# Kernel tuning notes

Measured on AMD Instinct MI355X. Metric: run time of the kernel, lower is better.

## Reference

```python
import jax, jax.numpy as jnp
import numpy as np
from jax import lax

B, M, T = 64, 90, 187
NNLS_ITERS = 500   # fixed-iteration FISTA projected-gradient NNLS (replaces scipy.optimize.nnls loop)
POWER_ITERS = 50
NEG = 0.33         # leaky_relu negative_slope in BrainNetCNN


def leaky(x):
    return jnp.where(x >= 0, x, NEG * x)


def setup_inputs() -> dict:
    key = jax.random.key(0)
    ks = jax.random.split(key, 18)
    f32 = jnp.float32
    def g(k, shape, scale=0.05):
        return jax.random.normal(k, shape, dtype=f32) * scale
    return {
        "x0_raw": jax.random.normal(ks[0], (B, M, T), dtype=f32),   # trunk output res0+res2
        "raw_x": jax.random.normal(ks[1], (B, M, T), dtype=f32),    # mel[:, 0]
        # BrainNetCNN(1, 90, 2) parameters (full-extent conv kernels stored without singleton dims)
        "cnn1_w": g(ks[2], (8, M)),   "cnn1_b": jnp.zeros((8,), f32),    # Conv2d(1,8,(1,90))
        "cnn2_w": g(ks[3], (8, M)),   "cnn2_b": jnp.zeros((8,), f32),    # Conv2d(1,8,(90,1))
        "cnn3_w": g(ks[4], (16, 8, M)), "cnn3_b": jnp.zeros((16,), f32), # Conv2d(8,16,(1,90))
        "cnn4_w": g(ks[5], (16, 8, M)), "cnn4_b": jnp.zeros((16,), f32), # Conv2d(8,16,(90,1))
        "e2n_w": g(ks[6], (16, M)),  "e2n_b": jnp.zeros((1,), f32),      # Conv2d(16,1,(1,90))
        "n2g_w": g(ks[7], (64, M)),  "n2g_b": jnp.zeros((64,), f32),     # Conv2d(1,64,(90,1))
        "d1_w": g(ks[8], (128, 64)), "d1_b": jnp.zeros((128,), f32),
        "d2_w": g(ks[9], (10, 128)), "d2_b": jnp.zeros((10,), f32),
        "d3_w": g(ks[10], (2, 10)),  "d3_b": jnp.zeros((2,), f32),
    }


def nnls_columns(x0_pred, raw_x):
    """Batched NNLS: for each (b, j) solve min_{w>=0} ||X[:, !=j] w - raw_x[b, j]||^2.
    X = x0_pred^T [B,T,M]. Column j is excluded via a mask (its coefficient is pinned to 0),
    which is equivalent to deleting the column. Returns A[b, j, m] with zero diagonal
    (matching torch: A[i, indx, j] = nnls(...); A = A.transpose(1,2))."""
    X = jnp.swapaxes(x0_pred, 1, 2)                    # [B,T,M]
    G = jnp.einsum('btm,btn->bmn', X, X)               # [B,M,M] Gram, shared over all j-problems
    C = jnp.einsum('btm,bjt->bjm', X, raw_x)           # [B,M(j),M] X^T b_j
    mask = 1.0 - jnp.eye(M, dtype=X.dtype)             # mask[j,m]: exclude column j
    # Lipschitz constant: top eigenvalue of G via power iteration (valid bound for masked subproblems)
    v = jnp.ones((G.shape[0], M), G.dtype)
    def pit(v, _):
        v = jnp.einsum('bmn,bn->bm', G, v)
        v = v / (jnp.linalg.norm(v, axis=1, keepdims=True) + 1e-12)
        return v, None
    v, _ = lax.scan(pit, v, None, length=POWER_ITERS)
    L = jnp.einsum('bm,bmn,bn->b', v, G, v) * 1.01 + 1e-8
    step = (1.0 / L)[:, None, None]
    w0 = jnp.zeros_like(C)
    def fista(carry, _):
        w, y, t = carry
        grad = (jnp.einsum('bmn,bjn->bjm', G, y) - C) * mask
        w1 = jnp.maximum(y - step * grad, 0.0)
        t1 = 0.5 * (1.0 + jnp.sqrt(1.0 + 4.0 * t * t))
        y1 = w1 + ((t - 1.0) / t1) * (w1 - w)
        return (w1, y1, t1), None
    (w, _, _), _ = lax.scan(fista, (w0, w0, jnp.float32(1.0)), None, length=NNLS_ITERS)
    return w  # [B, j, m], diag == 0


def brainnet_cnn(A, cnn1_w, cnn1_b, cnn2_w, cnn2_b, cnn3_w, cnn3_b, cnn4_w, cnn4_b,
                 e2n_w, e2n_b, n2g_w, n2g_b, d1_w, d1_b, d2_w, d2_b, d3_w, d3_b):
    # E2E layer 1: row conv broadcast over width + col conv broadcast over height
    a = jnp.einsum('bhw,ow->boh', A, cnn1_w) + cnn1_b[None, :, None]   # [B,8,90]
    b = jnp.einsum('bhw,oh->bow', A, cnn2_w) + cnn2_b[None, :, None]   # [B,8,90]
    o1 = leaky(a[:, :, :, None] + b[:, :, None, :])                    # [B,8,90,90]
    a2 = jnp.einsum('bchw,ocw->boh', o1, cnn3_w) + cnn3_b[None, :, None]
    b2 = jnp.einsum('bchw,och->bow', o1, cnn4_w) + cnn4_b[None, :, None]
    o2 = leaky(a2[:, :, :, None] + b2[:, :, None, :])                  # [B,16,90,90]
    e2n = leaky(jnp.einsum('bchw,cw->bh', o2, e2n_w) + e2n_b)          # [B,90]
    n2g = leaky(jnp.einsum('bh,oh->bo', e2n, n2g_w) + n2g_b)           # [B,64]
    h = leaky(n2g @ d1_w.T + d1_b)
    h = leaky(h @ d2_w.T + d2_b)
    return leaky(h @ d3_w.T + d3_b)                                    # [B,2]


def reference(x0_raw, raw_x, cnn1_w, cnn1_b, cnn2_w, cnn2_b, cnn3_w, cnn3_b, cnn4_w, cnn4_b,
              e2n_w, e2n_b, n2g_w, n2g_b, d1_w, d1_b, d2_w, d2_b, d3_w, d3_b):
    mean_v = jnp.mean(x0_raw, axis=(1, 2), keepdims=True)
    max_v = jnp.max(jnp.abs(x0_raw), axis=(1, 2), keepdims=True)
    x0_pred = (x0_raw - mean_v) / max_v
    # torch detaches NNLS inputs (.detach().numpy()); mirror with stop_gradient
    A = nnls_columns(lax.stop_gradient(x0_pred), lax.stop_gradient(raw_x))
    cls_pred = brainnet_cnn(A, cnn1_w, cnn1_b, cnn2_w, cnn2_b, cnn3_w, cnn3_b, cnn4_w, cnn4_b,
                            e2n_w, e2n_b, n2g_w, n2g_b, d1_w, d1_b, d2_w, d2_b, d3_w, d3_b)
    return (x0_pred[:, None, :, :], A, cls_pred)
```

## Files before the change

### kernel.cpp

```cpp
#include <hip/hip_runtime.h>
#include <math.h>


#define B_ 64
#define M_ 90
#define T_ 187
#define MP 96
#define NNLS_ITERS 500
#define POWER_ITERS 50
#define NEG_SLOPE 0.33f

#define MT_ (M_ * T_)
#define X0_OFF 0
#define A_OFF (B_ * MT_)
#define CLS_OFF (A_OFF + B_ * M_ * M_)

#define WS_G 0
#define WS_C (B_ * MP * MP)
#define WS_STEP (2 * B_ * MP * MP)
#define WS_W3R (WS_STEP + B_)
#define WS_W4R (WS_W3R + 16 * 8 * M_)

typedef float f32x4 __attribute__((ext_vector_type(4)));
typedef short s16x8 __attribute__((ext_vector_type(8)));

__device__ __forceinline__ float leaky(float x) {
    return x >= 0.f ? x : NEG_SLOPE * x;
}

__global__ __launch_bounds__(256) void k_norm(const float* __restrict__ x0,
                                              float* __restrict__ out) {
    int b = blockIdx.x, tid = threadIdx.x;
    const float* x = x0 + b * MT_;
    float s = 0.f, mx = 0.f;
    for (int i = tid; i < MT_; i += 256) {
        float v = x[i];
        s += v;
        mx = fmaxf(mx, fabsf(v));
    }
    __shared__ float rs[256], rm[256];
    rs[tid] = s; rm[tid] = mx;
    __syncthreads();
    for (int st = 128; st > 0; st >>= 1) {
        if (tid < st) {
            rs[tid] += rs[tid + st];
            rm[tid] = fmaxf(rm[tid], rm[tid + st]);
        }
        __syncthreads();
    }
    float mean = rs[0] / (float)MT_;
    float mv = rm[0];
    float* o = out + X0_OFF + b * MT_;
    for (int i = tid; i < MT_; i += 256) {
        o[i] = (x[i] - mean) / mv;
    }
}

#define TSTR 193
__global__ __launch_bounds__(256) void k_gc(const float* __restrict__ out_x0,
                                            const float* __restrict__ rawx,
                                            float* __restrict__ ws) {
    int b = blockIdx.x, nh = blockIdx.y, tid = threadIdx.x;
    __shared__ float Ps[MP * TSTR];
    __shared__ float Rs[48 * TSTR];

    for (int i = tid; i < MP * TSTR; i += 256) Ps[i] = 0.f;
    for (int i = tid; i < 48 * TSTR; i += 256) Rs[i] = 0.f;
    __syncthreads();

    const float* P = out_x0 + X0_OFF + b * MT_;
    const float* R = rawx + b * MT_;
    for (int i = tid; i < MT_; i += 256) {
        int m = i / T_, t = i - m * T_;
        Ps[m * TSTR + t] = P[i];
    }
    for (int i = tid; i < 48 * T_; i += 256) {
        int k = i / T_, t = i - k * T_;
        int r = nh * 48 + k;
        if (r < M_) Rs[k * TSTR + t] = R[r * T_ + t];
    }
    __syncthreads();

    int tn = tid & 15;
    int tm = tid >> 4;
    const float* pmp = &Ps[(tm * 6) * TSTR];
    const float* pnp = &Ps[(nh * 48 + tn * 3) * TSTR];
    const float* rnp = &Rs[(tn * 3) * TSTR];

    float accG[6][3], accC[6][3];
#pragma unroll
    for (int i = 0; i < 6; ++i)
#pragma unroll
        for (int k = 0; k < 3; ++k) { accG[i][k] = 0.f; accC[i][k] = 0.f; }

#pragma unroll 2
    for (int t = 0; t < T_; ++t) {
        float pm[6], pn[3], rn[3];
#pragma unroll
        for (int i = 0; i < 6; ++i) pm[i] = pmp[i * TSTR + t];
#pragma unroll
        for (int k = 0; k < 3; ++k) { pn[k] = pnp[k * TSTR + t]; rn[k] = rnp[k * TSTR + t]; }
#pragma unroll
        for (int i = 0; i < 6; ++i)
#pragma unroll
            for (int k = 0; k < 3; ++k) {
                accG[i][k] = fmaf(pm[i], pn[k], accG[i][k]);
                accC[i][k] = fmaf(pm[i], rn[k], accC[i][k]);
            }
    }

    float* G = ws + WS_G + b * MP * MP;
    float* C = ws + WS_C + b * MP * MP;
#pragma unroll
    for (int i = 0; i < 6; ++i)
#pragma unroll
        for (int k = 0; k < 3; ++k) {
            int m = tm * 6 + i;
            int n = nh * 48 + tn * 3 + k;
            G[m * MP + n] = accG[i][k];
            C[n * MP + m] = accC[i][k];
        }
}

__global__ __launch_bounds__(256) void k_prepack(const float* __restrict__ w3,
                                                 const float* __restrict__ w4,
                                                 float* __restrict__ ws) {
    int tid = threadIdx.x + blockIdx.x * 256;
    for (int i = tid; i < 16 * 8 * M_; i += 512) {
        int o = i & 15;
        int cw = i >> 4;
        int c = cw / M_;
        int w = cw % M_;
        ws[WS_W3R + i] = w3[(o * 8 + c) * M_ + w];
        ws[WS_W4R + i] = w4[(o * 8 + c) * M_ + w];
    }
}

#define GSTR 100
__global__ __launch_bounds__(64) void k_power(float* __restrict__ ws) {
    int b = blockIdx.x, lane = threadIdx.x;
    const float* Gg = ws + WS_G + b * MP * MP;
    __shared__ float Gs[MP * GSTR];
    __shared__ float vs[MP];

    for (int i = lane; i < MP * MP; i += 64) {
        int m = i / MP, n = i - m * MP;
        Gs[m * GSTR + n] = Gg[i];
    }
    vs[lane] = (lane < M_) ? 1.f : 0.f;
    if (lane < 32) vs[64 + lane] = (64 + lane < M_) ? 1.f : 0.f;

    const float4* g0 = (const float4*)&Gs[lane * GSTR];
    const float4* g1 = (const float4*)&Gs[(64 + (lane & 31)) * GSTR];
    const float4* v4 = (const float4*)vs;

    float r0 = 0.f, r1 = 0.f;
    for (int it = 0; it <= POWER_ITERS; ++it) {
        r0 = 0.f; r1 = 0.f;
#pragma unroll 6
        for (int k = 0; k < MP / 4; ++k) {
            float4 gv = g0[k];
            float4 vv = v4[k];
            r0 = fmaf(gv.x, vv.x, r0);
            r0 = fmaf(gv.y, vv.y, r0);
            r0 = fmaf(gv.z, vv.z, r0);
            r0 = fmaf(gv.w, vv.w, r0);
        }
        if (lane < 32) {
#pragma unroll 6
            for (int k = 0; k < MP / 4; ++k) {
                float4 gv = g1[k];
                float4 vv = v4[k];
                r1 = fmaf(gv.x, vv.x, r1);
                r1 = fmaf(gv.y, vv.y, r1);
                r1 = fmaf(gv.z, vv.z, r1);
                r1 = fmaf(gv.w, vv.w, r1);
            }
        }
        if (it == POWER_ITERS) break;
        float s = r0 * r0 + ((lane < 32) ? r1 * r1 : 0.f);
#pragma unroll
        for (int d = 1; d < 64; d <<= 1) s += __shfl_xor(s, d, 64);
        float inv = 1.f / (sqrtf(s) + 1e-12f);
        vs[lane] = r0 * inv;
        if (lane < 32) vs[64 + lane] = r1 * inv;
    }
    float s = vs[lane] * r0 + ((lane < 32) ? vs[64 + lane] * r1 : 0.f);
#pragma unroll
    for (int d = 1; d < 64; d <<= 1) s += __shfl_xor(s, d, 64);
    if (lane == 0) ws[WS_STEP + b] = 1.f / (s * 1.01f + 1e-8f);
}

#define YSTR 104

__global__ __launch_bounds__(192) void k_fista(const float* __restrict__ ws,
                                               float* __restrict__ out) {
    int b = blockIdx.y;
    int j0 = blockIdx.x * 16;
    int tid = threadIdx.x;
    int wid = tid >> 6;
    int lane = tid & 63;
    int jl = lane & 15;
    int g = lane >> 4;

    const float* Gg = ws + WS_G + b * MP * MP;
    const float* Cg = ws + WS_C + b * MP * MP;
    float step = ws[WS_STEP + b];

    __shared__ unsigned short Yt[2][2][16 * YSTR];

    for (int i = tid; i < 2 * 2 * 16 * YSTR / 2; i += 192)
        ((unsigned int*)Yt)[i] = 0u;

    s16x8 ghi[2][3], glo[2][3];
#pragma unroll
    for (int ml = 0; ml < 2; ++ml)
#pragma unroll
        for (int nc = 0; nc < 3; ++nc) {
            const float* src = Gg + ((wid * 2 + ml) * 16 + jl) * MP + nc * 32 + g * 8;
            s16x8 h, l;
#pragma unroll
            for (int e = 0; e < 8; ++e) {
                float f = src[e];
                unsigned int hb = __float_as_uint(f) & 0xFFFF0000u;
                h[e] = (short)(hb >> 16);
                float lo = f - __uint_as_float(hb);
                l[e] = (short)(__float_as_uint(lo) >> 16);
            }
            ghi[ml][nc] = h;
            glo[ml][nc] = l;
        }

    float c[2][4], w[2][4], y[2][4];
#pragma unroll
    for (int ml = 0; ml < 2; ++ml) {
        const float* src = Cg + (j0 + jl) * MP + (wid * 2 + ml) * 16 + g * 4;
#pragma unroll
        for (int r = 0; r < 4; ++r) {
            c[ml][r] = src[r];
            w[ml][r] = 0.f;
            y[ml][r] = 0.f;
        }
    }

    const unsigned short* rb[2][2];
    unsigned short* wb[2][2];
#pragma unroll
    for (int bu = 0; bu < 2; ++bu)
#pragma unroll
        for (int hl = 0; hl < 2; ++hl) {
            rb[bu][hl] = &Yt[bu][hl][jl * YSTR + g * 8];
            wb[bu][hl] = &Yt[bu][hl][jl * YSTR + wid * 32 + g * 4];
        }

    float t = 1.f;
    __syncthreads();

#define FISTA_BODY(CUR, NXT)                                                   \
    {                                                                          \
        s16x8 yh[3], yl[3];                                                    \
        _Pragma("unroll")                                                      \
        for (int nc = 0; nc < 3; ++nc) {                                       \
            yh[nc] = *(const s16x8*)(rb[CUR][0] + nc * 32);                    \
            yl[nc] = *(const s16x8*)(rb[CUR][1] + nc * 32);                    \
        }                                                                      \
        float t1 = 0.5f * (1.f + sqrtf(1.f + 4.f * t * t));                    \
        float coef = (t - 1.f) / t1;                                           \
        t = t1;                                                                \
        _Pragma("unroll")                                                      \
        for (int ml = 0; ml < 2; ++ml) {                                       \
            f32x4 a1 = {0.f, 0.f, 0.f, 0.f}, a2 = {0.f, 0.f, 0.f, 0.f};        \
            _Pragma("unroll")                                                  \
            for (int nc = 0; nc < 3; ++nc)                                     \
                a1 = __builtin_amdgcn_mfma_f32_16x16x32_bf16(ghi[ml][nc], yh[nc], a1, 0, 0, 0); \
            _Pragma("unroll")                                                  \
            for (int nc = 0; nc < 3; ++nc) {                                   \
                a2 = __builtin_amdgcn_mfma_f32_16x16x32_bf16(ghi[ml][nc], yl[nc], a2, 0, 0, 0); \
                a2 = __builtin_amdgcn_mfma_f32_16x16x32_bf16(glo[ml][nc], yh[nc], a2, 0, 0, 0); \
            }                                                                  \
            unsigned int hb[4], lb[4];                                         \
            _Pragma("unroll")                                                  \
            for (int r = 0; r < 4; ++r) {                                      \
                int mg = (wid * 2 + ml) * 16 + g * 4 + r;                      \
                float gr = (a1[r] + a2[r]) - c[ml][r];                         \
                if (j0 + jl == mg) gr = 0.f;                                   \
                float w1v = fmaxf(fmaf(-step, gr, y[ml][r]), 0.f);             \
                float yn = fmaf(coef, w1v - w[ml][r], w1v);                    \
                w[ml][r] = w1v;                                                \
                y[ml][r] = yn;                                                 \
                hb[r] = __float_as_uint(yn) & 0xFFFF0000u;                     \
                float lo = yn - __uint_as_float(hb[r]);                        \
                lb[r] = __float_as_uint(lo);                                   \
            }                                                                  \
            unsigned int h0 = (hb[0] >> 16) | hb[1];                           \
            unsigned int h1 = (hb[2] >> 16) | hb[3];                           \
            unsigned int l0 = (lb[0] >> 16) | (lb[1] & 0xFFFF0000u);           \
            unsigned int l1 = (lb[2] >> 16) | (lb[3] & 0xFFFF0000u);           \
            *(uint2*)(wb[NXT][0] + ml * 16) = make_uint2(h0, h1);              \
            *(uint2*)(wb[NXT][1] + ml * 16) = make_uint2(l0, l1);              \
        }                                                                      \
        __syncthreads();                                                       \
    }

    for (int it = 0; it < NNLS_ITERS / 2; ++it) {
        FISTA_BODY(0, 1)
        FISTA_BODY(1, 0)
    }
#undef FISTA_BODY

    int jg = j0 + jl;
#pragma unroll
    for (int ml = 0; ml < 2; ++ml)
#pragma unroll
        for (int r = 0; r < 4; ++r) {
            int mg = (wid * 2 + ml) * 16 + g * 4 + r;
            if (jg < M_ && mg < M_)
                out[A_OFF + b * M_ * M_ + jg * M_ + mg] = w[ml][r];
        }
}

__global__ __launch_bounds__(256) void k_cnn(
    const float* __restrict__ out_in, const float* __restrict__ ws,
    const float* __restrict__ c1w, const float* __restrict__ c1b,
    const float* __restrict__ c2w, const float* __restrict__ c2b,
    const float* __restrict__ c3b, const float* __restrict__ c4b,
    const float* __restrict__ e2nw, const float* __restrict__ e2nb,
    const float* __restrict__ n2gw, const float* __restrict__ n2gb,
    const float* __restrict__ d1w, const float* __restrict__ d1b,
    const float* __restrict__ d2w, const float* __restrict__ d2b,
    const float* __restrict__ d3w, const float* __restrict__ d3b,
    float* __restrict__ out) {
    int b = blockIdx.x, tid = threadIdx.x;
    __shared__ float A[M_][92];
    __shared__ float a1[8][92], b1[8][92];
    __shared__ float a2s[16][92], b2s[16][92];
    __shared__ float part[16][92];
    __shared__ float e2n[92], n2g[64], h1[128], h2[12];

    const float* Ag = out_in + A_OFF + b * M_ * M_;
    for (int i = tid; i < M_ * M_; i += 256) A[i / M_][i % M_] = Ag[i];
    __syncthreads();

    for (int q = tid; q < 8 * M_; q += 256) {
        int o = q & 7, h = q >> 3;
        float s = c1b[o];
#pragma unroll 2
        for (int wI = 0; wI < M_; ++wI) s = fmaf(A[h][wI], c1w[o * M_ + wI], s);
        a1[o][h] = s;
    }
    for (int q = tid; q < 8 * M_; q += 256) {
        int o = q & 7, wI = q >> 3;
        float s = c2b[o];
#pragma unroll 2
        for (int h = 0; h < M_; ++h) s = fmaf(A[h][wI], c2w[o * M_ + h], s);
        b1[o][wI] = s;
    }
    __syncthreads();

    const float4* w3r4 = (const float4*)(ws + WS_W3R);
    const float4* w4r4 = (const float4*)(ws + WS_W4R);
    for (int q = tid; q < 720; q += 256) {
        if (q < 360) {
            int oq = q & 3, h = q >> 2;
            float4 acc = make_float4(c3b[4 * oq], c3b[4 * oq + 1],
                                     c3b[4 * oq + 2], c3b[4 * oq + 3]);
#pragma unroll
            for (int ci = 0; ci < 8; ++ci) {
                float av = a1[ci][h];
                for (int wI = 0; wI < M_; ++wI) {
                    float o1v = leaky(av + b1[ci][wI]);
                    float4 wv = w3r4[(ci * M_ + wI) * 4 + oq];
                    acc.x = fmaf(o1v, wv.x, acc.x);
                    acc.y = fmaf(o1v, wv.y, acc.y);
                    acc.z = fmaf(o1v, wv.z, acc.z);
                    acc.w = fmaf(o1v, wv.w, acc.w);
                }
            }
            a2s[4 * oq + 0][h] = acc.x;
            a2s[4 * oq + 1][h] = acc.y;
            a2s[4 * oq + 2][h] = acc.z;
            a2s[4 * oq + 3][h] = acc.w;
        } else {
            int q2 = q - 360;
            int oq = q2 & 3, wI = q2 >> 2;
            float4 acc = make_float4(c4b[4 * oq], c4b[4 * oq + 1],
                                     c4b[4 * oq + 2], c4b[4 * oq + 3]);
#pragma unroll
            for (int ci = 0; ci < 8; ++ci) {
                float bv = b1[ci][wI];
                for (int h = 0; h < M_; ++h) {
                    float o1v = leaky(a1[ci][h] + bv);
                    float4 wv = w4r4[(ci * M_ + h) * 4 + oq];
                    acc.x = fmaf(o1v, wv.x, acc.x);
                    acc.y = fmaf(o1v, wv.y, acc.y);
                    acc.z = fmaf(o1v, wv.z, acc.z);
                    acc.w = fmaf(o1v, wv.w, acc.w);
                }
            }
            b2s[4 * oq + 0][wI] = acc.x;
            b2s[4 * oq + 1][wI] = acc.y;
            b2s[4 * oq + 2][wI] = acc.z;
            b2s[4 * oq + 3][wI] = acc.w;
        }
    }
    __syncthreads();

    for (int q = tid; q < 16 * M_; q += 256) {
        int ci = q & 15, h = q >> 4;
        float av = a2s[ci][h];
        float s = 0.f;
        for (int wI = 0; wI < M_; ++wI)
            s = fmaf(leaky(av + b2s[ci][wI]), e2nw[ci * M_ + wI], s);
        part[ci][h] = s;
    }
    __syncthreads();
    if (tid < M_) {
        float s = e2nb[0];
#pragma unroll
        for (int ci = 0; ci < 16; ++ci) s += part[ci][tid];
        e2n[tid] = leaky(s);
    }
    __syncthreads();
    if (tid < 64) {
        float s = n2gb[tid];
        for (int h = 0; h < M_; ++h) s = fmaf(e2n[h], n2gw[tid * M_ + h], s);
        n2g[tid] = leaky(s);
    }
    __syncthreads();
    if (tid < 128) {
        float s = d1b[tid];
        for (int k = 0; k < 64; ++k) s = fmaf(n2g[k], d1w[tid * 64 + k], s);
        h1[tid] = leaky(s);
    }
    __syncthreads();
    if (tid < 10) {
        float s = d2b[tid];
        for (int k = 0; k < 128; ++k) s = fmaf(h1[k], d2w[tid * 128 + k], s);
        h2[tid] = leaky(s);
    }
    __syncthreads();
    if (tid < 2) {
        float s = d3b[tid];
        for (int k = 0; k < 10; ++k) s = fmaf(h2[k], d3w[tid * 10 + k], s);
        out[CLS_OFF + b * 2 + tid] = leaky(s);
    }
}

extern "C" void kernel_launch(void* const* d_in, const int* in_sizes, int n_in,
                              void* d_out, int out_size, void* d_ws, size_t ws_size,
                              hipStream_t stream) {
    const float* x0 = (const float*)d_in[0];
    const float* rawx = (const float*)d_in[1];
    const float* c1w = (const float*)d_in[2];
    const float* c1b = (const float*)d_in[3];
    const float* c2w = (const float*)d_in[4];
    const float* c2b = (const float*)d_in[5];
    const float* c3w = (const float*)d_in[6];
    const float* c3b = (const float*)d_in[7];
    const float* c4w = (const float*)d_in[8];
    const float* c4b = (const float*)d_in[9];
    const float* e2nw = (const float*)d_in[10];
    const float* e2nb = (const float*)d_in[11];
    const float* n2gw = (const float*)d_in[12];
    const float* n2gb = (const float*)d_in[13];
    const float* d1w = (const float*)d_in[14];
    const float* d1b = (const float*)d_in[15];
    const float* d2w = (const float*)d_in[16];
    const float* d2b = (const float*)d_in[17];
    const float* d3w = (const float*)d_in[18];
    const float* d3b = (const float*)d_in[19];

    float* out = (float*)d_out;
    float* ws = (float*)d_ws;

    hipLaunchKernelGGL(k_norm, dim3(B_), dim3(256), 0, stream, x0, out);
    hipLaunchKernelGGL(k_gc, dim3(B_, 2), dim3(256), 0, stream, out, rawx, ws);
    hipLaunchKernelGGL(k_prepack, dim3(2), dim3(256), 0, stream, c3w, c4w, ws);
    hipLaunchKernelGGL(k_power, dim3(B_), dim3(64), 0, stream, ws);
    hipLaunchKernelGGL(k_fista, dim3(MP / 16, B_), dim3(192), 0, stream, ws, out);
    hipLaunchKernelGGL(k_cnn, dim3(B_), dim3(256), 0, stream, out, ws,
                       c1w, c1b, c2w, c2b, c3b, c4b, e2nw, e2nb,
                       n2gw, n2gb, d1w, d1b, d2w, d2b, d3w, d3b, out);
}
```

Measured before the change: 724.7 us.

## Fuse normalization into Gram kernel and split FISTA rows across six waves

Folds the per-batch normalization kernel into the Gram/cross-product kernel: each block recomputes the mean and max itself, and only the first column-half block writes x0_pred. This removes one launch and a global round-trip. The FISTA kernel now runs with 384 threads, so each wave owns a single 16-row tile instead of two. That halves the serial MFMA chain per iteration and splits the error-compensation MFMAs into three independent accumulators, in exchange for redundant reduction work and more waves contending at each per-iteration barrier.

```diff
diff --git a/kernel.cpp b/kernel.cpp
--- a/kernel.cpp
+++ b/kernel.cpp
@@ -28,18 +28,26 @@
     return x >= 0.f ? x : NEG_SLOPE * x;
 }
 
-__global__ __launch_bounds__(256) void k_norm(const float* __restrict__ x0,
-                                              float* __restrict__ out) {
-    int b = blockIdx.x, tid = threadIdx.x;
+#define TSTR 193
+__global__ __launch_bounds__(256) void k_gc(const float* __restrict__ x0,
+                                            const float* __restrict__ rawx,
+                                            float* __restrict__ ws,
+                                            float* __restrict__ out) {
+    int b = blockIdx.x, nh = blockIdx.y, tid = threadIdx.x;
+    __shared__ float Ps[MP * TSTR];
+    __shared__ float Rs[48 * TSTR];
+    __shared__ float rs[256], rm[256];
+
     const float* x = x0 + b * MT_;
-    float s = 0.f, mx = 0.f;
-    for (int i = tid; i < MT_; i += 256) {
-        float v = x[i];
-        s += v;
-        mx = fmaxf(mx, fabsf(v));
-    }
-    __shared__ float rs[256], rm[256];
-    rs[tid] = s; rm[tid] = mx;
+    {
+        float s = 0.f, mx = 0.f;
+        for (int i = tid; i < MT_; i += 256) {
+            float v = x[i];
+            s += v;
+            mx = fmaxf(mx, fabsf(v));
+        }
+        rs[tid] = s; rm[tid] = mx;
+    }
     __syncthreads();
     for (int st = 128; st > 0; st >>= 1) {
         if (tid < st) {
@@ -50,29 +58,18 @@
     }
     float mean = rs[0] / (float)MT_;
     float mv = rm[0];
+
+    for (int i = tid; i < MP * TSTR; i += 256) Ps[i] = 0.f;
+    for (int i = tid; i < 48 * TSTR; i += 256) Rs[i] = 0.f;
+    __syncthreads();
+
+    const float* R = rawx + b * MT_;
     float* o = out + X0_OFF + b * MT_;
     for (int i = tid; i < MT_; i += 256) {
-        o[i] = (x[i] - mean) / mv;
-    }
-}
-
-#define TSTR 193
-__global__ __launch_bounds__(256) void k_gc(const float* __restrict__ out_x0,
-                                            const float* __restrict__ rawx,
-                                            float* __restrict__ ws) {
-    int b = blockIdx.x, nh = blockIdx.y, tid = threadIdx.x;
-    __shared__ float Ps[MP * TSTR];
-    __shared__ float Rs[48 * TSTR];
-
-    for (int i = tid; i < MP * TSTR; i += 256) Ps[i] = 0.f;
-    for (int i = tid; i < 48 * TSTR; i += 256) Rs[i] = 0.f;
-    __syncthreads();
-
-    const float* P = out_x0 + X0_OFF + b * MT_;
-    const float* R = rawx + b * MT_;
-    for (int i = tid; i < MT_; i += 256) {
         int m = i / T_, t = i - m * T_;
-        Ps[m * TSTR + t] = P[i];
+        float pv = (x[i] - mean) / mv;
+        Ps[m * TSTR + t] = pv;
+        if (nh == 0) o[i] = pv;
     }
     for (int i = tid; i < 48 * T_; i += 256) {
         int k = i / T_, t = i - k * T_;
@@ -193,7 +190,7 @@
 
 #define YSTR 104
 
-__global__ __launch_bounds__(192) void k_fista(const float* __restrict__ ws,
+__global__ __launch_bounds__(384) void k_fista(const float* __restrict__ ws,
                                                float* __restrict__ out) {
     int b = blockIdx.y;
     int j0 = blockIdx.x * 16;
@@ -209,37 +206,34 @@
 
     __shared__ unsigned short Yt[2][2][16 * YSTR];
 
-    for (int i = tid; i < 2 * 2 * 16 * YSTR / 2; i += 192)
+    for (int i = tid; i < 2 * 2 * 16 * YSTR / 2; i += 384)
         ((unsigned int*)Yt)[i] = 0u;
 
-    s16x8 ghi[2][3], glo[2][3];
-#pragma unroll
-    for (int ml = 0; ml < 2; ++ml)
-#pragma unroll
-        for (int nc = 0; nc < 3; ++nc) {
-            const float* src = Gg + ((wid * 2 + ml) * 16 + jl) * MP + nc * 32 + g * 8;
-            s16x8 h, l;
-#pragma unroll
-            for (int e = 0; e < 8; ++e) {
-                float f = src[e];
-                unsigned int hb = __float_as_uint(f) & 0xFFFF0000u;
-                h[e] = (short)(hb >> 16);
-                float lo = f - __uint_as_float(hb);
-                l[e] = (short)(__float_as_uint(lo) >> 16);
-            }
-            ghi[ml][nc] = h;
-            glo[ml][nc] = l;
-        }
-
-    float c[2][4], w[2][4], y[2][4];
-#pragma unroll
-    for (int ml = 0; ml < 2; ++ml) {
-        const float* src = Cg + (j0 + jl) * MP + (wid * 2 + ml) * 16 + g * 4;
+    s16x8 ghi[3], glo[3];
+#pragma unroll
+    for (int nc = 0; nc < 3; ++nc) {
+        const float* src = Gg + (wid * 16 + jl) * MP + nc * 32 + g * 8;
+        s16x8 h, l;
+#pragma unroll
+        for (int e = 0; e < 8; ++e) {
+            float f = src[e];
+            unsigned int hb = __float_as_uint(f) & 0xFFFF0000u;
+            h[e] = (short)(hb >> 16);
+            float lo = f - __uint_as_float(hb);
+            l[e] = (short)(__float_as_uint(lo) >> 16);
+        }
+        ghi[nc] = h;
+        glo[nc] = l;
+    }
+
+    float c[4], w[4], y[4];
+    {
+        const float* src = Cg + (j0 + jl) * MP + wid * 16 + g * 4;
 #pragma unroll
         for (int r = 0; r < 4; ++r) {
-            c[ml][r] = src[r];
-            w[ml][r] = 0.f;
-            y[ml][r] = 0.f;
+            c[r] = src[r];
+            w[r] = 0.f;
+            y[r] = 0.f;
         }
     }
 
@@ -250,7 +244,7 @@
 #pragma unroll
         for (int hl = 0; hl < 2; ++hl) {
             rb[bu][hl] = &Yt[bu][hl][jl * YSTR + g * 8];
-            wb[bu][hl] = &Yt[bu][hl][jl * YSTR + wid * 32 + g * 4];
+            wb[bu][hl] = &Yt[bu][hl][jl * YSTR + wid * 16 + g * 4];
         }
 
     float t = 1.f;
@@ -267,38 +261,38 @@
         float t1 = 0.5f * (1.f + sqrtf(1.f + 4.f * t * t));                    \
         float coef = (t - 1.f) / t1;                                           \
         t = t1;                                                                \
+        f32x4 a1 = {0.f, 0.f, 0.f, 0.f};                                       \
+        f32x4 a2 = {0.f, 0.f, 0.f, 0.f};                                       \
+        f32x4 a3 = {0.f, 0.f, 0.f, 0.f};                                       \
         _Pragma("unroll")                                                      \
-        for (int ml = 0; ml < 2; ++ml) {                                       \
-            f32x4 a1 = {0.f, 0.f, 0.f, 0.f}, a2 = {0.f, 0.f, 0.f, 0.f};        \
-            _Pragma("unroll")                                                  \
-            for (int nc = 0; nc < 3; ++nc)                                     \
-                a1 = __builtin_amdgcn_mfma_f32_16x16x32_bf16(ghi[ml][nc], yh[nc], a1, 0, 0, 0); \
-            _Pragma("unroll")                                                  \
-            for (int nc = 0; nc < 3; ++nc) {                                   \
-                a2 = __builtin_amdgcn_mfma_f32_16x16x32_bf16(ghi[ml][nc], yl[nc], a2, 0, 0, 0); \
-                a2 = __builtin_amdgcn_mfma_f32_16x16x32_bf16(glo[ml][nc], yh[nc], a2, 0, 0, 0); \
-            }                                                                  \
-            unsigned int hb[4], lb[4];                                         \
-            _Pragma("unroll")                                                  \
-            for (int r = 0; r < 4; ++r) {                                      \
-                int mg = (wid * 2 + ml) * 16 + g * 4 + r;                      \
-                float gr = (a1[r] + a2[r]) - c[ml][r];                         \
-                if (j0 + jl == mg) gr = 0.f;                                   \
-                float w1v = fmaxf(fmaf(-step, gr, y[ml][r]), 0.f);             \
-                float yn = fmaf(coef, w1v - w[ml][r], w1v);                    \
-                w[ml][r] = w1v;                                                \
-                y[ml][r] = yn;                                                 \
-                hb[r] = __float_as_uint(yn) & 0xFFFF0000u;                     \
-                float lo = yn - __uint_as_float(hb[r]);                        \
-                lb[r] = __float_as_uint(lo);                                   \
-            }                                                                  \
-            unsigned int h0 = (hb[0] >> 16) | hb[1];                           \
-            unsigned int h1 = (hb[2] >> 16) | hb[3];                           \
-            unsigned int l0 = (lb[0] >> 16) | (lb[1] & 0xFFFF0000u);           \
-            unsigned int l1 = (lb[2] >> 16) | (lb[3] & 0xFFFF0000u);           \
-            *(uint2*)(wb[NXT][0] + ml * 16) = make_uint2(h0, h1);              \
-            *(uint2*)(wb[NXT][1] + ml * 16) = make_uint2(l0, l1);              \
+        for (int nc = 0; nc < 3; ++nc)                                         \
+            a1 = __builtin_amdgcn_mfma_f32_16x16x32_bf16(ghi[nc], yh[nc], a1, 0, 0, 0); \
+        _Pragma("unroll")                                                      \
+        for (int nc = 0; nc < 3; ++nc)                                         \
+            a2 = __builtin_amdgcn_mfma_f32_16x16x32_bf16(ghi[nc], yl[nc], a2, 0, 0, 0); \
+        _Pragma("unroll")                                                      \
+        for (int nc = 0; nc < 3; ++nc)                                         \
+            a3 = __builtin_amdgcn_mfma_f32_16x16x32_bf16(glo[nc], yh[nc], a3, 0, 0, 0); \
+        unsigned int hb[4], lb[4];                                             \
+        _Pragma("unroll")                                                      \
+        for (int r = 0; r < 4; ++r) {                                          \
+            int mg = wid * 16 + g * 4 + r;                                     \
+            float gr = (a1[r] + a2[r] + a3[r]) - c[r];                         \
+            if (j0 + jl == mg) gr = 0.f;                                       \
+            float w1v = fmaxf(fmaf(-step, gr, y[r]), 0.f);                     \
+            float yn = fmaf(coef, w1v - w[r], w1v);                            \
+            w[r] = w1v;                                                        \
+            y[r] = yn;                                                         \
+            hb[r] = __float_as_uint(yn) & 0xFFFF0000u;                         \
+            float lo = yn - __uint_as_float(hb[r]);                            \
+            lb[r] = __float_as_uint(lo);                                       \
         }                                                                      \
+        unsigned int h0 = (hb[0] >> 16) | hb[1];                               \
+        unsigned int h1 = (hb[2] >> 16) | hb[3];                               \
+        unsigned int l0 = (lb[0] >> 16) | (lb[1] & 0xFFFF0000u);               \
+        unsigned int l1 = (lb[2] >> 16) | (lb[3] & 0xFFFF0000u);               \
+        *(uint2*)(wb[NXT][0]) = make_uint2(h0, h1);                            \
+        *(uint2*)(wb[NXT][1]) = make_uint2(l0, l1);                            \
         __syncthreads();                                                       \
     }
 
@@ -310,13 +304,11 @@
 
     int jg = j0 + jl;
 #pragma unroll
-    for (int ml = 0; ml < 2; ++ml)
-#pragma unroll
-        for (int r = 0; r < 4; ++r) {
-            int mg = (wid * 2 + ml) * 16 + g * 4 + r;
-            if (jg < M_ && mg < M_)
-                out[A_OFF + b * M_ * M_ + jg * M_ + mg] = w[ml][r];
-        }
+    for (int r = 0; r < 4; ++r) {
+        int mg = wid * 16 + g * 4 + r;
+        if (jg < M_ && mg < M_)
+            out[A_OFF + b * M_ * M_ + jg * M_ + mg] = w[r];
+    }
 }
 
 __global__ __launch_bounds__(256) void k_cnn(
@@ -473,11 +465,10 @@
     float* out = (float*)d_out;
     float* ws = (float*)d_ws;
 
-    hipLaunchKernelGGL(k_norm, dim3(B_), dim3(256), 0, stream, x0, out);
-    hipLaunchKernelGGL(k_gc, dim3(B_, 2), dim3(256), 0, stream, out, rawx, ws);
+    hipLaunchKernelGGL(k_gc, dim3(B_, 2), dim3(256), 0, stream, x0, rawx, ws, out);
     hipLaunchKernelGGL(k_prepack, dim3(2), dim3(256), 0, stream, c3w, c4w, ws);
     hipLaunchKernelGGL(k_power, dim3(B_), dim3(64), 0, stream, ws);
-    hipLaunchKernelGGL(k_fista, dim3(MP / 16, B_), dim3(192), 0, stream, ws, out);
+    hipLaunchKernelGGL(k_fista, dim3(MP / 16, B_), dim3(384), 0, stream, ws, out);
     hipLaunchKernelGGL(k_cnn, dim3(B_), dim3(256), 0, stream, out, ws,
                        c1w, c1b, c2w, c2b, c3b, c4b, e2nw, e2nb,
                        n2gw, n2gb, d1w, d1b, d2w, d2b, d3w, d3b, out);
```

Measured after the change: 713.7 us. No clear change (-1.5%).
